# Kernel tuning notes

Measured on AMD Instinct MI355X. Metric: run time of the kernel, lower is better.

The kernel has to match this reference:

```python
import jax, jax.numpy as jnp
import numpy as np

IN_CHANNELS = 64
N_NODES = 100000
N_POOLED = 50000
N_EDGES = 1250000


def setup_inputs() -> dict:
    key = jax.random.key(0)
    k1, k2, k3 = jax.random.split(key, 3)
    x_abstract = jax.random.normal(k1, (N_POOLED, IN_CHANNELS), dtype=jnp.float32)
    # pooling indices: unique subset of [0, N)
    perm = jax.random.permutation(k2, N_NODES)[:N_POOLED].astype(jnp.int32)
    edge_index = jax.random.randint(k3, (2, N_EDGES), 0, N_NODES, dtype=jnp.int32)
    return {
        "x_abstract": x_abstract,
        "perm": perm,
        "edge_index": edge_index,
        "original_num_nodes": N_NODES,
    }


def reference(x_abstract, perm, edge_index, original_num_nodes):
    N = original_num_nodes
    C = x_abstract.shape[1]
    # scatter pooled features back to original node slots
    x0 = jnp.zeros((N, C), dtype=x_abstract.dtype).at[perm].set(x_abstract)
    is_missing = jnp.ones((N,), dtype=bool).at[perm].set(False)

    # undirected view: every edge contributes both directions
    tgt = jnp.concatenate([edge_index[0], edge_index[1]])  # [2E]
    src = jnp.concatenate([edge_index[1], edge_index[0]])  # [2E]

    # deduplicate (tgt, src) pairs (torch.unique on neighbor ids) via lexsort + adjacent-diff mask
    order = jnp.lexsort((src, tgt))
    t_s = tgt[order]
    s_s = src[order]
    uniq = jnp.concatenate(
        [jnp.array([True]), (t_s[1:] != t_s[:-1]) | (s_s[1:] != s_s[:-1])]
    )
    # drop self loops (neighbor_ids != idx), weight 1 for each unique neighbor pair
    w = (uniq & (t_s != s_s)).astype(x_abstract.dtype)  # [2E]

    # scatter-mean of unique-neighbor features per target node
    feat_sum = jax.ops.segment_sum(x0[s_s] * w[:, None], t_s, num_segments=N)  # [N, C]
    cnt = jax.ops.segment_sum(w, t_s, num_segments=N)  # [N]
    mean = feat_sum / jnp.maximum(cnt, 1.0)[:, None]

    # only missing nodes with at least one neighbor get filled; others keep their value
    fill = is_missing & (cnt > 0)
    return jnp.where(fill[:, None], mean, x0)
```

## Files before the change

kernel.cpp:

```cpp
#include <hip/hip_runtime.h>
#include <stdint.h>

#define K_SLOTS 64

__global__ void scatter_kernel(const float* __restrict__ xab,
                               const int* __restrict__ perm,
                               float* __restrict__ out,
                               int* __restrict__ inv,
                               int Np, int C4) {
    int gid = blockIdx.x * blockDim.x + threadIdx.x;
    int j = gid / C4;
    int q = gid - j * C4;
    if (j >= Np) return;
    int p = perm[j];
    if (q == 0) inv[p] = j;
    const float4* src = (const float4*)xab + (size_t)j * C4;
    float4* dst = (float4*)out + (size_t)p * C4;
    dst[q] = src[q];
}

__global__ void mklist_kernel(const int* __restrict__ inv,
                              int* __restrict__ work,
                              unsigned* __restrict__ wn, int N) {
    int i = blockIdx.x * blockDim.x + threadIdx.x;
    int lane = threadIdx.x & 63;
    bool miss = (i < N) && (inv[i] < 0);
    unsigned long long m = __ballot(miss);
    unsigned base = 0;
    if (lane == 0 && m) base = atomicAdd(wn, (unsigned)__popcll(m));
    base = __shfl((int)base, 0, 64);
    if (miss) {
        unsigned long long mask_lt = (1ull << lane) - 1ull;
        work[base + __popcll(m & mask_lt)] = i;
    }
}

__global__ void fill_kernel(const int* __restrict__ ei, long long E,
                            const int* __restrict__ inv,
                            int* __restrict__ deg,
                            int* __restrict__ slot) {
    long long e = (long long)blockIdx.x * blockDim.x + threadIdx.x;
    if (e >= E) return;
    int a = ei[e];
    int b = ei[e + E];
    if (a == b) return;
    if (inv[a] < 0) {
        int pos = atomicAdd(&deg[a], 1);
        if (pos < K_SLOTS) slot[((size_t)a << 6) + pos] = b;
    }
    if (inv[b] < 0) {
        int pos = atomicAdd(&deg[b], 1);
        if (pos < K_SLOTS) slot[((size_t)b << 6) + pos] = a;
    }
}

__global__ void mean_kernel(const int* __restrict__ work,
                            const int* __restrict__ slot,
                            const int* __restrict__ deg,
                            const int* __restrict__ inv,
                            const float* __restrict__ xab,
                            float* __restrict__ out,
                            int M, int C) {
    int wid = (int)((blockIdx.x * (long long)blockDim.x + threadIdx.x) >> 6);
    int lane = threadIdx.x & 63;
    if (wid >= M) return;
    int node = __builtin_amdgcn_readfirstlane(work[wid]);
    int d = deg[node];
    if (d > K_SLOTS) d = K_SLOTS;
    if (d <= 0) {
        for (int c = lane; c < C; c += 64) out[(size_t)node * C + c] = 0.0f;
        return;
    }
    int s = -1, j = -1;
    if (lane < d) {
        s = slot[((size_t)node << 6) + lane];
        j = inv[s];
    }
    bool dup = false;
    for (int k = 0; k < d - 1; ++k) {
        int v = __shfl(s, k, 64);
        if (lane > k && s == v) dup = true;
    }
    bool uniq = (lane < d) && !dup;
    int cnt = __popcll(__ballot(uniq));
    unsigned long long pm = __ballot(uniq && j >= 0);
    float rcnt = 1.0f / (float)cnt;
    for (int c0 = 0; c0 < C; c0 += 64) {
        int c = c0 + lane;
        bool cc = (c < C);
        float acc = 0.0f;
        unsigned long long m = pm;
        while (m) {
            int u0 = (int)__ffsll(m) - 1; m &= m - 1;
            int u1 = 0, u2 = 0, u3 = 0;
            bool h1 = (m != 0); if (h1) { u1 = (int)__ffsll(m) - 1; m &= m - 1; }
            bool h2 = (m != 0); if (h2) { u2 = (int)__ffsll(m) - 1; m &= m - 1; }
            bool h3 = (m != 0); if (h3) { u3 = (int)__ffsll(m) - 1; m &= m - 1; }
            int j0 = __shfl(j, u0, 64);
            int j1 = __shfl(j, u1, 64);
            int j2 = __shfl(j, u2, 64);
            int j3 = __shfl(j, u3, 64);
            float v0 = cc        ? xab[(size_t)j0 * C + c] : 0.0f;
            float v1 = (cc & h1) ? xab[(size_t)j1 * C + c] : 0.0f;
            float v2 = (cc & h2) ? xab[(size_t)j2 * C + c] : 0.0f;
            float v3 = (cc & h3) ? xab[(size_t)j3 * C + c] : 0.0f;
            acc += v0 + v1 + v2 + v3;
        }
        if (cc) out[(size_t)node * C + c] = acc * rcnt;
    }
}

extern "C" void kernel_launch(void* const* d_in, const int* in_sizes, int n_in,
                              void* d_out, int out_size, void* d_ws, size_t ws_size,
                              hipStream_t stream) {
    const float* xab  = (const float*)d_in[0];
    const int*   perm = (const int*)d_in[1];
    const int*   ei   = (const int*)d_in[2];
    float* out = (float*)d_out;

    int Np = in_sizes[1];
    int C  = in_sizes[0] / Np;
    long long E = in_sizes[2] / 2;
    int N  = out_size / C;
    int C4 = C / 4;
    int M  = N - Np;

    char* ws = (char*)d_ws;
    size_t off = 0;
    int* slot = (int*)(ws + off); off += (size_t)N * K_SLOTS * 4;
    int* deg  = (int*)(ws + off); off += (size_t)N * 4;
    int* inv  = (int*)(ws + off); off += (size_t)N * 4;
    int* work = (int*)(ws + off); off += (size_t)M * 4;
    unsigned* wn = (unsigned*)(ws + off); off += 256;

    hipMemsetAsync(deg, 0, (size_t)N * 4, stream);
    hipMemsetAsync(inv, 0xFF, (size_t)N * 4, stream);
    hipMemsetAsync(wn, 0, 4, stream);

    {
        long long threads = (long long)Np * C4;
        int blocks = (int)((threads + 255) / 256);
        scatter_kernel<<<blocks, 256, 0, stream>>>(xab, perm, out, inv, Np, C4);
    }
    {
        int blocks = (N + 255) / 256;
        mklist_kernel<<<blocks, 256, 0, stream>>>(inv, work, wn, N);
    }
    {
        int blocks = (int)((E + 255) / 256);
        fill_kernel<<<blocks, 256, 0, stream>>>(ei, E, inv, deg, slot);
    }
    {
        long long threads = (long long)M * 64;
        int blocks = (int)((threads + 255) / 256);
        mean_kernel<<<blocks, 256, 0, stream>>>(work, slot, deg, inv, xab, out, M, C);
    }
}
```

Measured before the change: 222.0 us.

## Partition nodes into 8 ranges mapped per XCD for fill and mean kernels

Splits nodes into 8 contiguous partitions and assigns blocks by blockIdx modulo 8, so each block works only on one partition. The aim is to keep the deg/slot atomics and the slot reads local to one XCD's L2 on MI355X. The fill kernel now resolves each neighbour's pooled index up front and stores it in the slot, so the mean kernel skips the dependent inv lookup. Inv is encoded with a +1 offset so a single memset clears both deg and inv. The cost is that every partition's blocks re-read the full edge list (about 8x the edge traffic), and the per-partition work lists add an extra grouping loop in mklist.

```diff
diff --git a/kernel.cpp b/kernel.cpp
--- a/kernel.cpp
+++ b/kernel.cpp
@@ -2,6 +2,7 @@
 #include <stdint.h>
 
 #define K_SLOTS 64
+#define NPART 8
 
 __global__ void scatter_kernel(const float* __restrict__ xab,
                                const int* __restrict__ perm,
@@ -13,7 +14,7 @@
     int q = gid - j * C4;
     if (j >= Np) return;
     int p = perm[j];
-    if (q == 0) inv[p] = j;
+    if (q == 0) inv[p] = j + 1;
     const float4* src = (const float4*)xab + (size_t)j * C4;
     float4* dst = (float4*)out + (size_t)p * C4;
     dst[q] = src[q];
@@ -21,69 +22,84 @@
 
 __global__ void mklist_kernel(const int* __restrict__ inv,
                               int* __restrict__ work,
-                              unsigned* __restrict__ wn, int N) {
+                              unsigned* __restrict__ wn8,
+                              int N, int pS, int CAPW) {
     int i = blockIdx.x * blockDim.x + threadIdx.x;
     int lane = threadIdx.x & 63;
-    bool miss = (i < N) && (inv[i] < 0);
-    unsigned long long m = __ballot(miss);
-    unsigned base = 0;
-    if (lane == 0 && m) base = atomicAdd(wn, (unsigned)__popcll(m));
-    base = __shfl((int)base, 0, 64);
-    if (miss) {
-        unsigned long long mask_lt = (1ull << lane) - 1ull;
-        work[base + __popcll(m & mask_lt)] = i;
+    bool miss = (i < N) && (inv[i] == 0);
+    int myp = (i < N) ? (i / pS) : 0;
+    unsigned long long rem = __ballot(miss);
+    while (rem) {
+        int lead = (int)__ffsll(rem) - 1;
+        int lp = __shfl(myp, lead, 64);
+        unsigned long long grp = __ballot(miss && (myp == lp));
+        unsigned base = 0;
+        if (lane == lead) base = atomicAdd(&wn8[lp], (unsigned)__popcll(grp));
+        base = (unsigned)__shfl((int)base, lead, 64);
+        if (miss && myp == lp)
+            work[(size_t)lp * CAPW + base + __popcll(grp & ((1ull << lane) - 1ull))] = i;
+        rem &= ~grp;
     }
 }
 
 __global__ void fill_kernel(const int* __restrict__ ei, long long E,
                             const int* __restrict__ inv,
                             int* __restrict__ deg,
-                            int* __restrict__ slot) {
-    long long e = (long long)blockIdx.x * blockDim.x + threadIdx.x;
-    if (e >= E) return;
-    int a = ei[e];
-    int b = ei[e + E];
-    if (a == b) return;
-    if (inv[a] < 0) {
-        int pos = atomicAdd(&deg[a], 1);
-        if (pos < K_SLOTS) slot[((size_t)a << 6) + pos] = b;
-    }
-    if (inv[b] < 0) {
-        int pos = atomicAdd(&deg[b], 1);
-        if (pos < K_SLOTS) slot[((size_t)b << 6) + pos] = a;
+                            int* __restrict__ slot,
+                            int pS, int N) {
+    int p = blockIdx.x & (NPART - 1);
+    int q = blockIdx.x >> 3;
+    int lo = p * pS;
+    int hi = lo + pS; if (hi > N) hi = N;
+    long long stride = (long long)(gridDim.x >> 3) * blockDim.x;
+    for (long long e = (long long)q * blockDim.x + threadIdx.x; e < E; e += stride) {
+        int a = __builtin_nontemporal_load(ei + e);
+        int b = __builtin_nontemporal_load(ei + e + E);
+        if (a == b) continue;
+        if (a >= lo && a < hi && inv[a] == 0) {
+            int ib = inv[b];
+            int enc = (ib > 0) ? (ib - 1) : (-1 - b);
+            int pos = atomicAdd(&deg[a], 1);
+            if (pos < K_SLOTS) slot[((size_t)a << 6) + pos] = enc;
+        }
+        if (b >= lo && b < hi && inv[b] == 0) {
+            int ia = inv[a];
+            int enc = (ia > 0) ? (ia - 1) : (-1 - a);
+            int pos = atomicAdd(&deg[b], 1);
+            if (pos < K_SLOTS) slot[((size_t)b << 6) + pos] = enc;
+        }
     }
 }
 
 __global__ void mean_kernel(const int* __restrict__ work,
+                            const unsigned* __restrict__ wn8,
                             const int* __restrict__ slot,
                             const int* __restrict__ deg,
-                            const int* __restrict__ inv,
                             const float* __restrict__ xab,
                             float* __restrict__ out,
-                            int M, int C) {
-    int wid = (int)((blockIdx.x * (long long)blockDim.x + threadIdx.x) >> 6);
+                            int CAPW, int C) {
+    int p = blockIdx.x & (NPART - 1);
+    int idx = (int)((blockIdx.x >> 3) * (blockDim.x >> 6) + (threadIdx.x >> 6));
     int lane = threadIdx.x & 63;
-    if (wid >= M) return;
-    int node = __builtin_amdgcn_readfirstlane(work[wid]);
+    unsigned live = wn8[p]; if (live > (unsigned)CAPW) live = CAPW;
+    if ((unsigned)idx >= live) return;
+    int node = __builtin_amdgcn_readfirstlane(work[(size_t)p * CAPW + idx]);
     int d = deg[node];
     if (d > K_SLOTS) d = K_SLOTS;
     if (d <= 0) {
         for (int c = lane; c < C; c += 64) out[(size_t)node * C + c] = 0.0f;
         return;
     }
-    int s = -1, j = -1;
-    if (lane < d) {
-        s = slot[((size_t)node << 6) + lane];
-        j = inv[s];
-    }
+    int e = -1;
+    if (lane < d) e = slot[((size_t)node << 6) + lane];
     bool dup = false;
     for (int k = 0; k < d - 1; ++k) {
-        int v = __shfl(s, k, 64);
-        if (lane > k && s == v) dup = true;
+        int v = __shfl(e, k, 64);
+        if (lane > k && e == v) dup = true;
     }
     bool uniq = (lane < d) && !dup;
     int cnt = __popcll(__ballot(uniq));
-    unsigned long long pm = __ballot(uniq && j >= 0);
+    unsigned long long pm = __ballot(uniq && e >= 0);
     float rcnt = 1.0f / (float)cnt;
     for (int c0 = 0; c0 < C; c0 += 64) {
         int c = c0 + lane;
@@ -96,10 +112,10 @@
             bool h1 = (m != 0); if (h1) { u1 = (int)__ffsll(m) - 1; m &= m - 1; }
             bool h2 = (m != 0); if (h2) { u2 = (int)__ffsll(m) - 1; m &= m - 1; }
             bool h3 = (m != 0); if (h3) { u3 = (int)__ffsll(m) - 1; m &= m - 1; }
-            int j0 = __shfl(j, u0, 64);
-            int j1 = __shfl(j, u1, 64);
-            int j2 = __shfl(j, u2, 64);
-            int j3 = __shfl(j, u3, 64);
+            int j0 = __shfl(e, u0, 64);
+            int j1 = __shfl(e, u1, 64);
+            int j2 = __shfl(e, u2, 64);
+            int j3 = __shfl(e, u3, 64);
             float v0 = cc        ? xab[(size_t)j0 * C + c] : 0.0f;
             float v1 = (cc & h1) ? xab[(size_t)j1 * C + c] : 0.0f;
             float v2 = (cc & h2) ? xab[(size_t)j2 * C + c] : 0.0f;
@@ -123,19 +139,18 @@
     long long E = in_sizes[2] / 2;
     int N  = out_size / C;
     int C4 = C / 4;
-    int M  = N - Np;
+    int pS = (N + NPART - 1) / NPART;
+    int CAPW = (pS + 63) & ~63;
 
     char* ws = (char*)d_ws;
     size_t off = 0;
     int* slot = (int*)(ws + off); off += (size_t)N * K_SLOTS * 4;
     int* deg  = (int*)(ws + off); off += (size_t)N * 4;
     int* inv  = (int*)(ws + off); off += (size_t)N * 4;
-    int* work = (int*)(ws + off); off += (size_t)M * 4;
-    unsigned* wn = (unsigned*)(ws + off); off += 256;
+    unsigned* wn8 = (unsigned*)(ws + off); off += 64 * 4;
+    int* work = (int*)(ws + off); off += (size_t)NPART * CAPW * 4;
 
-    hipMemsetAsync(deg, 0, (size_t)N * 4, stream);
-    hipMemsetAsync(inv, 0xFF, (size_t)N * 4, stream);
-    hipMemsetAsync(wn, 0, 4, stream);
+    hipMemsetAsync(deg, 0, ((size_t)2 * N + 64) * 4, stream);
 
     {
         long long threads = (long long)Np * C4;
@@ -144,15 +159,12 @@
     }
     {
         int blocks = (N + 255) / 256;
-        mklist_kernel<<<blocks, 256, 0, stream>>>(inv, work, wn, N);
+        mklist_kernel<<<blocks, 256, 0, stream>>>(inv, work, wn8, N, pS, CAPW);
     }
+    fill_kernel<<<8 * 1024, 256, 0, stream>>>(ei, E, inv, deg, slot, pS, N);
     {
-        int blocks = (int)((E + 255) / 256);
-        fill_kernel<<<blocks, 256, 0, stream>>>(ei, E, inv, deg, slot);
-    }
-    {
-        long long threads = (long long)M * 64;
-        int blocks = (int)((threads + 255) / 256);
-        mean_kernel<<<blocks, 256, 0, stream>>>(work, slot, deg, inv, xab, out, M, C);
+        int blocksPerP = (CAPW + 3) / 4;
+        mean_kernel<<<NPART * blocksPerP, 256, 0, stream>>>(work, wn8, slot, deg,
+                                                            xab, out, CAPW, C);
     }
 }
```

New measurement: 237.8 us. 1.07x slower.
